# Kernel tuning notes

Measured on AMD Instinct MI355X. Metric: run time of the kernel, lower is better.

## Reference

```python
import jax, jax.numpy as jnp
import numpy as np

T = 4194304  # sequence length (2**22)

def setup_inputs() -> dict:
    key = jax.random.key(0)
    k = jax.random.split(key, 7)
    return {
        "x_0": jax.random.normal(k[0], (1, 2), dtype=jnp.float32),
        "u": jax.random.normal(k[1], (2, T), dtype=jnp.float32),
        "timedelta": jax.random.uniform(k[2], (T,), dtype=jnp.float32),
        # scale W_A down so the linear recurrence x_t = A x_{t-1} + ... is stable over 4M steps
        "W_A": 0.3 * jax.random.normal(k[3], (2, 2), dtype=jnp.float32),
        "b_A": 0.1 * jax.random.normal(k[4], (2,), dtype=jnp.float32),
        "W_B": jax.random.normal(k[5], (2, 2), dtype=jnp.float32),
        "b_B": 0.1 * jax.random.normal(k[6], (2,), dtype=jnp.float32),
    }

def reference(x_0, u, timedelta, W_A, b_A, W_B, b_B):
    # forward_PINN: linear state recurrence x_t = A x_{t-1} + B u_t (+biases),
    # output_t = physics_prediction(x_{t-1}, u_t, dt_t) - x_t
    x0 = x_0[0]          # [2] state (x, y)
    u_seq = u.T          # [T, 2] controls (speed, heading)

    def step(x_prev, inp):
        u_t, dt = inp                                  # [2], scalar
        x_t = W_A @ x_prev + b_A + W_B @ u_t + b_B     # [2]
        c = u_t[0] * dt
        pinn = x_prev + jnp.stack([c * jnp.cos(u_t[1]), c * jnp.sin(u_t[1])])
        return x_t, pinn - x_t

    _, x_out = jax.lax.scan(step, x0, (u_seq, timedelta))  # [T, 2]
    return x_out
```

## Files before the change

kernel.cpp:

```cpp
#include <hip/hip_runtime.h>

#define T_TOTAL 4194304
#define S 16
#define NTHREADS 256
#define BLOCK_T (NTHREADS * S)
#define HALO_SEG 4
#define NSEG (NTHREADS + HALO_SEG)
#define NSEG_PAD (NSEG + 1)
#define NSTAGE (NSEG * S)

struct M22 { float m00, m01, m10, m11; };
__device__ __forceinline__ M22 mmul(const M22& X, const M22& Y) {
    M22 r;
    r.m00 = fmaf(X.m00, Y.m00, X.m01 * Y.m10);
    r.m01 = fmaf(X.m00, Y.m01, X.m01 * Y.m11);
    r.m10 = fmaf(X.m10, Y.m00, X.m11 * Y.m10);
    r.m11 = fmaf(X.m10, Y.m01, X.m11 * Y.m11);
    return r;
}

__global__ __launch_bounds__(NTHREADS)
void pinn_rnn_kernel(const float* __restrict__ x0p,
                     const float* __restrict__ u,
                     const float* __restrict__ td,
                     const float* __restrict__ WA,
                     const float* __restrict__ bA,
                     const float* __restrict__ WB,
                     const float* __restrict__ bB,
                     float* __restrict__ out)
{
    __shared__ float2 lu [S][NSEG_PAD];
    __shared__ float  ldt[S][NSEG_PAD];
    __shared__ float2 lc [NSEG];

    const int tid = threadIdx.x;
    const int B0  = blockIdx.x * BLOCK_T;

    const float a00 = WA[0], a01 = WA[1], a10 = WA[2], a11 = WA[3];
    const float w00 = WB[0], w01 = WB[1], w10 = WB[2], w11 = WB[3];
    const float bc0 = bA[0] + bB[0];
    const float bc1 = bA[1] + bB[1];

    const float* u0 = u;
    const float* u1 = u + T_TOTAL;

    for (int i = tid; i < NSTAGE; i += NTHREADS) {
        int t = B0 - HALO_SEG * S + i;
        float ua = 0.f, ub = 0.f, dtv = 0.f;
        if (t >= 0) { ua = u0[t]; ub = u1[t]; dtv = td[t]; }
        int seg = i >> 4, j = i & (S - 1);
        lu [j][seg] = make_float2(ua, ub);
        ldt[j][seg] = dtv;
    }

    M22 A  = { a00, a01, a10, a11 };
    M22 A2 = mmul(A,  A );
    M22 A4 = mmul(A2, A2);
    M22 A8 = mmul(A4, A4);
    M22 M  = mmul(A8, A8);
    M22 M2 = mmul(M,  M );
    M22 M3 = mmul(M2, M );

    __syncthreads();

    const int g = tid + HALO_SEG;

    {
        float x0v = 0.f, x1v = 0.f;
        #pragma unroll
        for (int j = 0; j < S; ++j) {
            float2 uu = lu[j][g];
            float v0 = fmaf(w00, uu.x, fmaf(w01, uu.y, bc0));
            float v1 = fmaf(w10, uu.x, fmaf(w11, uu.y, bc1));
            float n0 = fmaf(a00, x0v, fmaf(a01, x1v, v0));
            float n1 = fmaf(a10, x0v, fmaf(a11, x1v, v1));
            x0v = n0; x1v = n1;
        }
        lc[g] = make_float2(x0v, x1v);
    }
    if (tid < HALO_SEG) {
        if (blockIdx.x == 0) {
            lc[tid] = make_float2(0.f, 0.f);
        } else {
            float x0v = 0.f, x1v = 0.f;
            #pragma unroll
            for (int j = 0; j < S; ++j) {
                float2 uu = lu[j][tid];
                float v0 = fmaf(w00, uu.x, fmaf(w01, uu.y, bc0));
                float v1 = fmaf(w10, uu.x, fmaf(w11, uu.y, bc1));
                float n0 = fmaf(a00, x0v, fmaf(a01, x1v, v0));
                float n1 = fmaf(a10, x0v, fmaf(a11, x1v, v1));
                x0v = n0; x1v = n1;
            }
            lc[tid] = make_float2(x0v, x1v);
        }
    }
    __syncthreads();

    float2 c1 = lc[g - 1], c2 = lc[g - 2], c3 = lc[g - 3], c4 = lc[g - 4];
    float xi0 = c1.x
              + fmaf(M.m00,  c2.x, M.m01  * c2.y)
              + fmaf(M2.m00, c3.x, M2.m01 * c3.y)
              + fmaf(M3.m00, c4.x, M3.m01 * c4.y);
    float xi1 = c1.y
              + fmaf(M.m10,  c2.x, M.m11  * c2.y)
              + fmaf(M2.m10, c3.x, M2.m11 * c3.y)
              + fmaf(M3.m10, c4.x, M3.m11 * c4.y);

    if (blockIdx.x == 0 && tid < HALO_SEG) {
        float X0 = x0p[0], X1 = x0p[1];
        M22 P;
        if      (tid == 0) { P.m00 = 1.f; P.m01 = 0.f; P.m10 = 0.f; P.m11 = 1.f; }
        else if (tid == 1) P = M;
        else if (tid == 2) P = M2;
        else               P = M3;
        xi0 += fmaf(P.m00, X0, P.m01 * X1);
        xi1 += fmaf(P.m10, X0, P.m11 * X1);
    }

    float x0v = xi0, x1v = xi1;
    const int aG = B0 + tid * S;
    float2* outp = (float2*)out;
    #pragma unroll
    for (int j = 0; j < S; ++j) {
        float2 uu = lu[j][g];
        float dtv = ldt[j][g];
        float v0 = fmaf(w00, uu.x, fmaf(w01, uu.y, bc0));
        float v1 = fmaf(w10, uu.x, fmaf(w11, uu.y, bc1));
        float n0 = fmaf(a00, x0v, fmaf(a01, x1v, v0));
        float n1 = fmaf(a10, x0v, fmaf(a11, x1v, v1));
        float cc = uu.x * dtv;
        float sn, cs;
        __sincosf(uu.y, &sn, &cs);
        outp[aG + j] = make_float2(fmaf(cc, cs, x0v) - n0,
                                   fmaf(cc, sn, x1v) - n1);
        x0v = n0; x1v = n1;
    }
}

extern "C" void kernel_launch(void* const* d_in, const int* in_sizes, int n_in,
                              void* d_out, int out_size, void* d_ws, size_t ws_size,
                              hipStream_t stream) {
    const float* x0p = (const float*)d_in[0];
    const float* u   = (const float*)d_in[1];
    const float* td  = (const float*)d_in[2];
    const float* WA  = (const float*)d_in[3];
    const float* bA  = (const float*)d_in[4];
    const float* WB  = (const float*)d_in[5];
    const float* bB  = (const float*)d_in[6];
    float* outp = (float*)d_out;

    dim3 grid(T_TOTAL / BLOCK_T);
    dim3 block(NTHREADS);
    pinn_rnn_kernel<<<grid, block, 0, stream>>>(x0p, u, td, WA, bA, WB, bB, outp);
}
```

Baseline: 125.2 us.

## Load inputs directly to registers with float4 and stage output through swizzled LDS

Each thread now loads its own 16 contiguous u0/u1/dt elements straight into registers with 128-bit vector loads, and halo threads load their halo segments themselves, so the LDS staging of the inputs goes away. Outputs are written to a swizzled shared buffer and then stored to global memory with coalesced float4 writes, replacing the strided per-thread float2 stores. Launch bounds now request 4 blocks per CU. The cost is higher register pressure from 48 input floats per thread, and the per-thread strided float4 loads may coalesce less well than the old staged loads.

```diff
diff --git a/kernel.cpp b/kernel.cpp
--- a/kernel.cpp
+++ b/kernel.cpp
@@ -6,8 +6,6 @@
 #define BLOCK_T (NTHREADS * S)
 #define HALO_SEG 4
 #define NSEG (NTHREADS + HALO_SEG)
-#define NSEG_PAD (NSEG + 1)
-#define NSTAGE (NSEG * S)
 
 struct M22 { float m00, m01, m10, m11; };
 __device__ __forceinline__ M22 mmul(const M22& X, const M22& Y) {
@@ -19,7 +17,17 @@
     return r;
 }
 
-__global__ __launch_bounds__(NTHREADS)
+struct alignas(16) F16 { float f[16]; };
+__device__ __forceinline__ void load16(F16& d, const float* __restrict__ p) {
+    const float4* q = (const float4*)p;
+    float4 a0 = q[0], a1 = q[1], a2 = q[2], a3 = q[3];
+    *(float4*)&d.f[0]  = a0;
+    *(float4*)&d.f[4]  = a1;
+    *(float4*)&d.f[8]  = a2;
+    *(float4*)&d.f[12] = a3;
+}
+
+__global__ __launch_bounds__(NTHREADS, 4)
 void pinn_rnn_kernel(const float* __restrict__ x0p,
                      const float* __restrict__ u,
                      const float* __restrict__ td,
@@ -29,9 +37,8 @@
                      const float* __restrict__ bB,
                      float* __restrict__ out)
 {
-    __shared__ float2 lu [S][NSEG_PAD];
-    __shared__ float  ldt[S][NSEG_PAD];
-    __shared__ float2 lc [NSEG];
+    __shared__ float2 lc[NSEG];
+    __shared__ float2 lout[BLOCK_T];
 
     const int tid = threadIdx.x;
     const int B0  = blockIdx.x * BLOCK_T;
@@ -44,97 +51,103 @@
     const float* u0 = u;
     const float* u1 = u + T_TOTAL;
 
-    for (int i = tid; i < NSTAGE; i += NTHREADS) {
-        int t = B0 - HALO_SEG * S + i;
-        float ua = 0.f, ub = 0.f, dtv = 0.f;
-        if (t >= 0) { ua = u0[t]; ub = u1[t]; dtv = td[t]; }
-        int seg = i >> 4, j = i & (S - 1);
-        lu [j][seg] = make_float2(ua, ub);
-        ldt[j][seg] = dtv;
-    }
+    const int t0 = B0 + tid * S;
+    F16 U0, U1, DT;
+    load16(U0, u0 + t0);
+    load16(U1, u1 + t0);
+    load16(DT, td + t0);
 
-    M22 A  = { a00, a01, a10, a11 };
-    M22 A2 = mmul(A,  A );
-    M22 A4 = mmul(A2, A2);
-    M22 A8 = mmul(A4, A4);
-    M22 M  = mmul(A8, A8);
-    M22 M2 = mmul(M,  M );
-    M22 M3 = mmul(M2, M );
-
-    __syncthreads();
-
-    const int g = tid + HALO_SEG;
+    M22 A   = { a00, a01, a10, a11 };
+    M22 A2  = mmul(A,  A );
+    M22 A4  = mmul(A2, A2);
+    M22 A8  = mmul(A4, A4);
+    M22 M   = mmul(A8, A8);
+    M22 Mp2 = mmul(M,  M );
+    M22 Mp3 = mmul(Mp2, M);
 
     {
         float x0v = 0.f, x1v = 0.f;
         #pragma unroll
         for (int j = 0; j < S; ++j) {
-            float2 uu = lu[j][g];
-            float v0 = fmaf(w00, uu.x, fmaf(w01, uu.y, bc0));
-            float v1 = fmaf(w10, uu.x, fmaf(w11, uu.y, bc1));
+            float v0 = fmaf(w00, U0.f[j], fmaf(w01, U1.f[j], bc0));
+            float v1 = fmaf(w10, U0.f[j], fmaf(w11, U1.f[j], bc1));
             float n0 = fmaf(a00, x0v, fmaf(a01, x1v, v0));
             float n1 = fmaf(a10, x0v, fmaf(a11, x1v, v1));
             x0v = n0; x1v = n1;
         }
-        lc[g] = make_float2(x0v, x1v);
+        lc[tid + HALO_SEG] = make_float2(x0v, x1v);
     }
     if (tid < HALO_SEG) {
-        if (blockIdx.x == 0) {
-            lc[tid] = make_float2(0.f, 0.f);
-        } else {
+        float2 ch = make_float2(0.f, 0.f);
+        if (blockIdx.x != 0) {
+            const int th = B0 - HALO_SEG * S + tid * S;
+            F16 H0, H1;
+            load16(H0, u0 + th);
+            load16(H1, u1 + th);
             float x0v = 0.f, x1v = 0.f;
             #pragma unroll
             for (int j = 0; j < S; ++j) {
-                float2 uu = lu[j][tid];
-                float v0 = fmaf(w00, uu.x, fmaf(w01, uu.y, bc0));
-                float v1 = fmaf(w10, uu.x, fmaf(w11, uu.y, bc1));
+                float v0 = fmaf(w00, H0.f[j], fmaf(w01, H1.f[j], bc0));
+                float v1 = fmaf(w10, H0.f[j], fmaf(w11, H1.f[j], bc1));
                 float n0 = fmaf(a00, x0v, fmaf(a01, x1v, v0));
                 float n1 = fmaf(a10, x0v, fmaf(a11, x1v, v1));
                 x0v = n0; x1v = n1;
             }
-            lc[tid] = make_float2(x0v, x1v);
+            ch = make_float2(x0v, x1v);
+        }
+        lc[tid] = ch;
+    }
+    __syncthreads();
+
+    float2 c1 = lc[tid + 3], c2 = lc[tid + 2], c3 = lc[tid + 1], c4 = lc[tid];
+    float xi0 = c1.x
+              + fmaf(M.m00,   c2.x, M.m01   * c2.y)
+              + fmaf(Mp2.m00, c3.x, Mp2.m01 * c3.y)
+              + fmaf(Mp3.m00, c4.x, Mp3.m01 * c4.y);
+    float xi1 = c1.y
+              + fmaf(M.m10,   c2.x, M.m11   * c2.y)
+              + fmaf(Mp2.m10, c3.x, Mp2.m11 * c3.y)
+              + fmaf(Mp3.m10, c4.x, Mp3.m11 * c4.y);
+
+    if (blockIdx.x == 0 && tid < HALO_SEG) {
+        float X0 = x0p[0], X1 = x0p[1];
+        M22 P;
+        if      (tid == 0) P = { 1.f, 0.f, 0.f, 1.f };
+        else if (tid == 1) P = M;
+        else if (tid == 2) P = Mp2;
+        else               P = Mp3;
+        xi0 += fmaf(P.m00, X0, P.m01 * X1);
+        xi1 += fmaf(P.m10, X0, P.m11 * X1);
+    }
+
+    {
+        const int xm = tid & 14;
+        float2* lrow = lout + tid * S;
+        float x0v = xi0, x1v = xi1;
+        #pragma unroll
+        for (int j = 0; j < S; ++j) {
+            float v0 = fmaf(w00, U0.f[j], fmaf(w01, U1.f[j], bc0));
+            float v1 = fmaf(w10, U0.f[j], fmaf(w11, U1.f[j], bc1));
+            float n0 = fmaf(a00, x0v, fmaf(a01, x1v, v0));
+            float n1 = fmaf(a10, x0v, fmaf(a11, x1v, v1));
+            float cc = U0.f[j] * DT.f[j];
+            float sn, cs;
+            __sincosf(U1.f[j], &sn, &cs);
+            lrow[j ^ xm] = make_float2(fmaf(cc, cs, x0v) - n0,
+                                       fmaf(cc, sn, x1v) - n1);
+            x0v = n0; x1v = n1;
         }
     }
     __syncthreads();
 
-    float2 c1 = lc[g - 1], c2 = lc[g - 2], c3 = lc[g - 3], c4 = lc[g - 4];
-    float xi0 = c1.x
-              + fmaf(M.m00,  c2.x, M.m01  * c2.y)
-              + fmaf(M2.m00, c3.x, M2.m01 * c3.y)
-              + fmaf(M3.m00, c4.x, M3.m01 * c4.y);
-    float xi1 = c1.y
-              + fmaf(M.m10,  c2.x, M.m11  * c2.y)
-              + fmaf(M2.m10, c3.x, M2.m11 * c3.y)
-              + fmaf(M3.m10, c4.x, M3.m11 * c4.y);
-
-    if (blockIdx.x == 0 && tid < HALO_SEG) {
-        float X0 = x0p[0], X1 = x0p[1];
-        M22 P;
-        if      (tid == 0) { P.m00 = 1.f; P.m01 = 0.f; P.m10 = 0.f; P.m11 = 1.f; }
-        else if (tid == 1) P = M;
-        else if (tid == 2) P = M2;
-        else               P = M3;
-        xi0 += fmaf(P.m00, X0, P.m01 * X1);
-        xi1 += fmaf(P.m10, X0, P.m11 * X1);
-    }
-
-    float x0v = xi0, x1v = xi1;
-    const int aG = B0 + tid * S;
-    float2* outp = (float2*)out;
+    const float4* lo4 = (const float4*)lout;
+    float4* og = (float4*)out + (B0 >> 1);
     #pragma unroll
-    for (int j = 0; j < S; ++j) {
-        float2 uu = lu[j][g];
-        float dtv = ldt[j][g];
-        float v0 = fmaf(w00, uu.x, fmaf(w01, uu.y, bc0));
-        float v1 = fmaf(w10, uu.x, fmaf(w11, uu.y, bc1));
-        float n0 = fmaf(a00, x0v, fmaf(a01, x1v, v0));
-        float n1 = fmaf(a10, x0v, fmaf(a11, x1v, v1));
-        float cc = uu.x * dtv;
-        float sn, cs;
-        __sincosf(uu.y, &sn, &cs);
-        outp[aG + j] = make_float2(fmaf(cc, cs, x0v) - n0,
-                                   fmaf(cc, sn, x1v) - n1);
-        x0v = n0; x1v = n1;
+    for (int m = 0; m < 8; ++m) {
+        int f    = m * NTHREADS + tid;
+        int i0   = f << 1;
+        int slot = i0 ^ ((i0 >> 4) & 14);
+        og[f] = lo4[slot >> 1];
     }
 }
 
```

After: 106.6 us. 1.17x faster.
